# Performance work log

Measured on AMD Instinct MI355X. Metric: run time of the kernel, lower is better.

## Reference

```python
import jax, jax.numpy as jnp
import numpy as np

B, T, V, H, NH, NLVL = 64, 2048, 256, 64, 4, 2
HD = H // NH  # 16
EPS = 1e-5


def setup_inputs() -> dict:
    key = jax.random.key(0)
    ks = jax.random.split(key, 16)
    s = 0.05
    return {
        "x": jax.random.randint(ks[0], (B, T), 0, V),
        "emb": jax.random.normal(ks[1], (V, H), dtype=jnp.float32) * s,
        # LSTM params, PyTorch gate order i, f, g, o stacked along dim 0
        "w_ih": jax.random.normal(ks[2], (4 * H, H), dtype=jnp.float32) * s,
        "w_hh": jax.random.normal(ks[3], (4 * H, H), dtype=jnp.float32) * s,
        "b_ih": jax.random.normal(ks[4], (4 * H,), dtype=jnp.float32) * s,
        "b_hh": jax.random.normal(ks[5], (4 * H,), dtype=jnp.float32) * s,
        # two MHA levels, packed qkv in_proj like nn.MultiheadAttention
        "wqkv": jax.random.normal(ks[6], (NLVL, 3 * H, H), dtype=jnp.float32) * s,
        "bqkv": jax.random.normal(ks[7], (NLVL, 3 * H), dtype=jnp.float32) * s,
        "wo": jax.random.normal(ks[8], (NLVL, H, H), dtype=jnp.float32) * s,
        "bo": jax.random.normal(ks[9], (NLVL, H), dtype=jnp.float32) * s,
        "ln_g": jnp.ones((H,), dtype=jnp.float32),
        "ln_b": jnp.zeros((H,), dtype=jnp.float32),
        "fc_w": jax.random.normal(ks[10], (V, H), dtype=jnp.float32) * s,
        "fc_b": jax.random.normal(ks[11], (V,), dtype=jnp.float32) * s,
    }


def _lstm(x, w_ih, w_hh, b_ih, b_hh):
    # x: (B, T, H) -> (B, T, H); single layer, PyTorch gate order i,f,g,o
    b = x.shape[0]
    h0 = jnp.zeros((b, H), x.dtype)
    c0 = jnp.zeros((b, H), x.dtype)

    def step(carry, xt):
        h, c = carry
        g = xt @ w_ih.T + b_ih + h @ w_hh.T + b_hh  # (B, 4H)
        i, f, gg, o = jnp.split(g, 4, axis=-1)
        c = jax.nn.sigmoid(f) * c + jax.nn.sigmoid(i) * jnp.tanh(gg)
        h = jax.nn.sigmoid(o) * jnpp_tanh(c) if False else jax.nn.sigmoid(o) * jnp.tanh(c)
        return (h, c), h

    _, hs = jax.lax.scan(step, (h0, c0), jnp.swapaxes(x, 0, 1))  # (T, B, H)
    return jnp.swapaxes(hs, 0, 1)


def _mha(x, wqkv, bqkv, wo, bo):
    # Faithful to nn.MultiheadAttention with batch_first=False:
    # x: (L, N, E) where here L = batch dim of lstm_out, N = seq dim.
    L, N, E = x.shape
    qkv = x @ wqkv.T + bqkv  # (L, N, 3E)
    q, k, v = jnp.split(qkv, 3, axis=-1)
    q = q.reshape(L, N, NH, HD)
    k = k.reshape(L, N, NH, HD)
    v = v.reshape(L, N, NH, HD)
    scale = jnp.asarray(1.0 / np.sqrt(HD), x.dtype)
    att = jax.nn.softmax(jnp.einsum('lnhd,mnhd->nhlm', q, k) * scale, axis=-1)
    o = jnp.einsum('nhlm,mnhd->lnhd', att, v).reshape(L, N, E)
    return o @ wo.T + bo


def reference(x, emb, w_ih, w_hh, b_ih, b_hh, wqkv, bqkv, wo, bo, ln_g, ln_b, fc_w, fc_b):
    h = emb[x]  # (B, T, H)
    h = _lstm(h, w_ih, w_hh, b_ih, b_hh)  # (B, T, H)
    for l in range(NLVL):
        h = _mha(h, wqkv[l], bqkv[l], wo[l], bo[l])
    mu = jnp.mean(h, axis=-1, keepdims=True)
    var = jnp.mean(jnp.square(h - mu), axis=-1, keepdims=True)  # biased, like torch LN
    hn = (h - mu) * jax.lax.rsqrt(var + EPS) * ln_g + ln_b
    return hn @ fc_w.T + fc_b  # (B, T, V)
```

## Files before the change

### kernel.cpp

```cpp
#include <hip/hip_runtime.h>

enum { TT = 2048, HH = 64, BB = 64, GG = 256, VV = 256 };

static __device__ __forceinline__ void bar_lds(){
  asm volatile("s_waitcnt lgkmcnt(0)\n\ts_barrier" ::: "memory");
}

__global__ __launch_bounds__(256) void k_embw(const float* __restrict__ emb,
                                              const float* __restrict__ w_ih,
                                              const float* __restrict__ b_ih,
                                              const float* __restrict__ b_hh,
                                              float* __restrict__ embW){
  int v = blockIdx.x, g = threadIdx.x;
  __shared__ float e[HH];
  if (g < HH) e[g] = emb[v*HH + g];
  bar_lds();
  float acc = b_ih[g] + b_hh[g];
  const float* wr = w_ih + g*HH;
#pragma unroll
  for (int k = 0; k < HH; k += 4){
    float4 w4 = *(const float4*)(wr + k);
    acc = fmaf(e[k],   w4.x, acc); acc = fmaf(e[k+1], w4.y, acc);
    acc = fmaf(e[k+2], w4.z, acc); acc = fmaf(e[k+3], w4.w, acc);
  }
  embW[v*GG + g] = acc;
}

__global__ __launch_bounds__(256) void k_lstm(const int* __restrict__ x,
                                              const float* __restrict__ embW,
                                              const float* __restrict__ w_hh,
                                              float* __restrict__ hout){
  int b = blockIdx.x, g = threadIdx.x;
  __shared__ float hsh[HH];
  __shared__ float gsh[GG];
  float w[HH];
  {
    const float* wr = w_hh + g*HH;
#pragma unroll
    for (int k = 0; k < HH; k += 4)
      *(float4*)&w[k] = *(const float4*)(wr + k);
  }
  if (g < HH) hsh[g] = 0.f;
  float c = 0.f;
  const int* xb = x + b*TT;
  int i0 = xb[0];
  float gx = embW[i0*GG + g];
  int i1 = xb[1];
  const bool istanh = ((g >> 6) == 2);
  float* houtb = hout + (size_t)b*TT*HH;
  bar_lds();
#pragma unroll 2
  for (int t = 0; t < TT; t++){
    float gxn = embW[i1*GG + g];
    int inx = xb[(t + 2 < TT) ? (t + 2) : (TT - 1)];
    float a0 = 0.f, a1 = 0.f, a2 = 0.f, a3 = 0.f;
#pragma unroll
    for (int k = 0; k < 16; k += 4){
      float4 h0 = *(const float4*)&hsh[k];
      float4 h1 = *(const float4*)&hsh[16 + k];
      float4 h2 = *(const float4*)&hsh[32 + k];
      float4 h3 = *(const float4*)&hsh[48 + k];
      a0 = fmaf(w[k],      h0.x, a0); a0 = fmaf(w[k+1],    h0.y, a0);
      a0 = fmaf(w[k+2],    h0.z, a0); a0 = fmaf(w[k+3],    h0.w, a0);
      a1 = fmaf(w[16+k],   h1.x, a1); a1 = fmaf(w[16+k+1], h1.y, a1);
      a1 = fmaf(w[16+k+2], h1.z, a1); a1 = fmaf(w[16+k+3], h1.w, a1);
      a2 = fmaf(w[32+k],   h2.x, a2); a2 = fmaf(w[32+k+1], h2.y, a2);
      a2 = fmaf(w[32+k+2], h2.z, a2); a2 = fmaf(w[32+k+3], h2.w, a2);
      a3 = fmaf(w[48+k],   h3.x, a3); a3 = fmaf(w[48+k+1], h3.y, a3);
      a3 = fmaf(w[48+k+2], h3.z, a3); a3 = fmaf(w[48+k+3], h3.w, a3);
    }
    float acc = ((a0 + a1) + (a2 + a3)) + gx;
    float val;
    if (istanh) val = 1.f - 2.f/(__expf(2.f*acc) + 1.f);
    else        val = 1.f/(1.f + __expf(-acc));
    gsh[g] = val;
    bar_lds();
    if (g < HH){
      float i_ = gsh[g], f_ = gsh[HH+g], gg = gsh[128+g], o_ = gsh[192+g];
      c = fmaf(f_, c, i_*gg);
      float th = 1.f - 2.f/(__expf(2.f*c) + 1.f);
      float hv = o_*th;
      hsh[g] = hv;
      houtb[(size_t)t*HH + g] = hv;
    }
    bar_lds();
    gx = gxn; i1 = inx;
  }
}

__global__ __launch_bounds__(256) void k_mha(const float* __restrict__ hin,
                                             const float* __restrict__ wqkv,
                                             const float* __restrict__ bqkv,
                                             const float* __restrict__ wo,
                                             const float* __restrict__ bo,
                                             float* __restrict__ hout){
  int t = blockIdx.x, tid = threadIdx.x;
  __shared__ float xta[BB][HH];
  __shared__ float qkvs[BB][192];

  float wq[HH]; float bq = 0.f;
  if (tid < 192){
#pragma unroll
    for (int k = 0; k < HH; k += 4)
      *(float4*)&wq[k] = *(const float4*)(wqkv + tid*HH + k);
    bq = bqkv[tid];
  }
  {
    int r = tid >> 2, q = tid & 3;
    const float* p = hin + (size_t)(r*TT + t)*HH + q*16;
#pragma unroll
    for (int j = 0; j < 16; j += 4)
      *(float4*)&xta[r][q*16 + j] = *(const float4*)(p + j);
  }
  bar_lds();
  if (tid < 192){
#pragma unroll 4
    for (int b = 0; b < BB; b++){
      float acc = bq;
#pragma unroll
      for (int k = 0; k < HH; k += 4){
        float4 xv = *(const float4*)&xta[b][k];
        acc = fmaf(wq[k],   xv.x, acc); acc = fmaf(wq[k+1], xv.y, acc);
        acc = fmaf(wq[k+2], xv.z, acc); acc = fmaf(wq[k+3], xv.w, acc);
      }
      qkvs[b][tid] = acc;
    }
  }
  bar_lds();
  {
    int hd = tid >> 6, l = tid & 63;
    int qo = hd*16, ko = 64 + hd*16, vo = 128 + hd*16;
    float4 q0 = *(const float4*)&qkvs[l][qo];
    float4 q1 = *(const float4*)&qkvs[l][qo+4];
    float4 q2 = *(const float4*)&qkvs[l][qo+8];
    float4 q3 = *(const float4*)&qkvs[l][qo+12];
    float S[BB];
#pragma unroll
    for (int m = 0; m < BB; m++){
      float4 k0 = *(const float4*)&qkvs[m][ko];
      float4 k1 = *(const float4*)&qkvs[m][ko+4];
      float4 k2 = *(const float4*)&qkvs[m][ko+8];
      float4 k3 = *(const float4*)&qkvs[m][ko+12];
      float d;
      d = q0.x*k0.x;         d = fmaf(q0.y,k0.y,d); d = fmaf(q0.z,k0.z,d); d = fmaf(q0.w,k0.w,d);
      d = fmaf(q1.x,k1.x,d); d = fmaf(q1.y,k1.y,d); d = fmaf(q1.z,k1.z,d); d = fmaf(q1.w,k1.w,d);
      d = fmaf(q2.x,k2.x,d); d = fmaf(q2.y,k2.y,d); d = fmaf(q2.z,k2.z,d); d = fmaf(q2.w,k2.w,d);
      d = fmaf(q3.x,k3.x,d); d = fmaf(q3.y,k3.y,d); d = fmaf(q3.z,k3.z,d); d = fmaf(q3.w,k3.w,d);
      S[m] = 0.25f*d;
    }
    float mx = S[0];
#pragma unroll
    for (int m = 1; m < BB; m++) mx = fmaxf(mx, S[m]);
    float sum = 0.f;
#pragma unroll
    for (int m = 0; m < BB; m++){ S[m] = __expf(S[m] - mx); sum += S[m]; }
    float inv = 1.f/sum;
    float4 a0 = make_float4(0,0,0,0), a1 = a0, a2 = a0, a3 = a0;
#pragma unroll
    for (int m = 0; m < BB; m++){
      float s = S[m];
      float4 v0 = *(const float4*)&qkvs[m][vo];
      float4 v1 = *(const float4*)&qkvs[m][vo+4];
      float4 v2 = *(const float4*)&qkvs[m][vo+8];
      float4 v3 = *(const float4*)&qkvs[m][vo+12];
      a0.x = fmaf(s,v0.x,a0.x); a0.y = fmaf(s,v0.y,a0.y); a0.z = fmaf(s,v0.z,a0.z); a0.w = fmaf(s,v0.w,a0.w);
      a1.x = fmaf(s,v1.x,a1.x); a1.y = fmaf(s,v1.y,a1.y); a1.z = fmaf(s,v1.z,a1.z); a1.w = fmaf(s,v1.w,a1.w);
      a2.x = fmaf(s,v2.x,a2.x); a2.y = fmaf(s,v2.y,a2.y); a2.z = fmaf(s,v2.z,a2.z); a2.w = fmaf(s,v2.w,a2.w);
      a3.x = fmaf(s,v3.x,a3.x); a3.y = fmaf(s,v3.y,a3.y); a3.z = fmaf(s,v3.z,a3.z); a3.w = fmaf(s,v3.w,a3.w);
    }
    a0.x*=inv; a0.y*=inv; a0.z*=inv; a0.w*=inv;
    a1.x*=inv; a1.y*=inv; a1.z*=inv; a1.w*=inv;
    a2.x*=inv; a2.y*=inv; a2.z*=inv; a2.w*=inv;
    a3.x*=inv; a3.y*=inv; a3.z*=inv; a3.w*=inv;
    bar_lds();
    *(float4*)&xta[l][qo]    = a0;
    *(float4*)&xta[l][qo+4]  = a1;
    *(float4*)&xta[l][qo+8]  = a2;
    *(float4*)&xta[l][qo+12] = a3;
  }
  bar_lds();
  {
    int c = tid & 63, wg = tid >> 6;
    float wor[HH];
#pragma unroll
    for (int k = 0; k < HH; k += 4)
      *(float4*)&wor[k] = *(const float4*)(wo + c*HH + k);
    float bo4 = bo[c];
#pragma unroll 2
    for (int j = 0; j < 16; j++){
      int b = wg*16 + j;
      float acc = bo4;
#pragma unroll
      for (int k = 0; k < HH; k += 4){
        float4 xv = *(const float4*)&xta[b][k];
        acc = fmaf(wor[k],   xv.x, acc); acc = fmaf(wor[k+1], xv.y, acc);
        acc = fmaf(wor[k+2], xv.z, acc); acc = fmaf(wor[k+3], xv.w, acc);
      }
      hout[(size_t)(b*TT + t)*HH + c] = acc;
    }
  }
}

__global__ __launch_bounds__(256) void k_fc(const float* __restrict__ hin,
                                            const float* __restrict__ ln_g,
                                            const float* __restrict__ ln_b,
                                            const float* __restrict__ fc_w,
                                            const float* __restrict__ fc_b,
                                            float* __restrict__ out){
  int tid = threadIdx.x;
  __shared__ float tile[64][68];
  __shared__ float ps[64][4];
  __shared__ float pq[64][4];
  __shared__ float mu[64], rs[64];
  float w[HH];
  float wsum = 0.f, bias2 = fc_b[tid];
#pragma unroll
  for (int k = 0; k < HH; k += 4){
    float4 wv = *(const float4*)(fc_w + tid*HH + k);
    float4 gv = *(const float4*)(ln_g + k);
    float4 bv = *(const float4*)(ln_b + k);
    bias2 = fmaf(bv.x, wv.x, bias2); bias2 = fmaf(bv.y, wv.y, bias2);
    bias2 = fmaf(bv.z, wv.z, bias2); bias2 = fmaf(bv.w, wv.w, bias2);
    w[k]   = gv.x*wv.x; w[k+1] = gv.y*wv.y;
    w[k+2] = gv.z*wv.z; w[k+3] = gv.w*wv.w;
    wsum += w[k] + w[k+1] + w[k+2] + w[k+3];
  }
  int r = tid >> 2, q = tid & 3;
  for (int ti = 0; ti < 4; ti++){
    int rowbase = blockIdx.x*256 + ti*64;
    const float* p = hin + (size_t)(rowbase + r)*HH + q*16;
    float xv[16];
#pragma unroll
    for (int j = 0; j < 16; j += 4)
      *(float4*)&xv[j] = *(const float4*)(p + j);
    float s1 = 0.f, s2 = 0.f;
#pragma unroll
    for (int j = 0; j < 16; j++){ s1 += xv[j]; s2 = fmaf(xv[j], xv[j], s2); }
#pragma unroll
    for (int j = 0; j < 16; j += 4)
      *(float4*)&tile[r][q*16 + j] = *(const float4*)&xv[j];
    ps[r][q] = s1; pq[r][q] = s2;
    bar_lds();
    if (tid < 64){
      float4 a  = *(const float4*)&ps[tid][0];
      float4 b4 = *(const float4*)&pq[tid][0];
      float m = (a.x + a.y + a.z + a.w) * (1.f/64.f);
      float v = (b4.x + b4.y + b4.z + b4.w) * (1.f/64.f) - m*m;
      mu[tid] = m;
      rs[tid] = rsqrtf(v + 1e-5f);
    }
    bar_lds();
#pragma unroll 2
    for (int rr = 0; rr < 64; rr++){
      float acc = 0.f;
#pragma unroll
      for (int k = 0; k < HH; k += 4){
        float4 x4 = *(const float4*)&tile[rr][k];
        acc = fmaf(w[k],   x4.x, acc); acc = fmaf(w[k+1], x4.y, acc);
        acc = fmaf(w[k+2], x4.z, acc); acc = fmaf(w[k+3], x4.w, acc);
      }
      float o = rs[rr]*(acc - mu[rr]*wsum) + bias2;
      out[(size_t)(rowbase + rr)*VV + tid] = o;
    }
    bar_lds();
  }
}

extern "C" void kernel_launch(void* const* d_in, const int* in_sizes, int n_in,
                              void* d_out, int out_size, void* d_ws, size_t ws_size,
                              hipStream_t stream){
  (void)in_sizes; (void)n_in; (void)out_size; (void)ws_size;
  const int*   x    = (const int*)d_in[0];
  const float* emb  = (const float*)d_in[1];
  const float* w_ih = (const float*)d_in[2];
  const float* w_hh = (const float*)d_in[3];
  const float* b_ih = (const float*)d_in[4];
  const float* b_hh = (const float*)d_in[5];
  const float* wqkv = (const float*)d_in[6];
  const float* bqkv = (const float*)d_in[7];
  const float* wo   = (const float*)d_in[8];
  const float* bo   = (const float*)d_in[9];
  const float* ln_g = (const float*)d_in[10];
  const float* ln_b = (const float*)d_in[11];
  const float* fc_w = (const float*)d_in[12];
  const float* fc_b = (const float*)d_in[13];

  char* ws = (char*)d_ws;
  float* embW = (float*)ws;
  float* bufA = (float*)(ws + (1<<20));
  float* bufB = bufA + (size_t)BB*TT*HH;

  k_embw<<<VV,  256, 0, stream>>>(emb, w_ih, b_ih, b_hh, embW);
  k_lstm<<<BB,  256, 0, stream>>>(x, embW, w_hh, bufA);
  k_mha <<<TT,  256, 0, stream>>>(bufA, wqkv,          bqkv,       wo,          bo,      bufB);
  k_mha <<<TT,  256, 0, stream>>>(bufB, wqkv + 192*64, bqkv + 192, wo + 64*64,  bo + 64, bufA);
  k_fc  <<<512, 256, 0, stream>>>(bufA, ln_g, ln_b, fc_w, fc_b, (float*)d_out);
}
```

Baseline: 1.775 ms.

## Batch 16 LSTM sequences per block and use bf16 MFMA for recurrence

The LSTM recurrence now processes 16 batch rows per block and computes the hidden-to-gate matmul with bf16 MFMA 16x16x32 instructions. The input-gate contribution seeds the accumulator. The weights are held as bf16 fragments in registers and the hidden state as bf16 in LDS. Each thread handles all four gates for its rows, which removes the gate-exchange barrier, but only 4 blocks are launched instead of 64. This trades parallelism across CUs and fp32 precision in the recurrent matmul for fewer serialized per-step instructions.

```diff
diff --git a/kernel.cpp b/kernel.cpp
--- a/kernel.cpp
+++ b/kernel.cpp
@@ -1,9 +1,24 @@
 #include <hip/hip_runtime.h>
 
 enum { TT = 2048, HH = 64, BB = 64, GG = 256, VV = 256 };
+
+typedef __attribute__((ext_vector_type(8))) short bf16x8;
+typedef __attribute__((ext_vector_type(4))) float f32x4;
 
 static __device__ __forceinline__ void bar_lds(){
   asm volatile("s_waitcnt lgkmcnt(0)\n\ts_barrier" ::: "memory");
+}
+
+static __device__ __forceinline__ unsigned short f2bs(float f){
+  unsigned int u = __builtin_bit_cast(unsigned int, f);
+  u += 0x7fffu + ((u >> 16) & 1u);
+  return (unsigned short)(u >> 16);
+}
+static __device__ __forceinline__ bf16x8 pack8(const float* v){
+  union { unsigned short s[8]; bf16x8 v8; } u;
+#pragma unroll
+  for (int i = 0; i < 8; i++) u.s[i] = f2bs(v[i]);
+  return u.v8;
 }
 
 __global__ __launch_bounds__(256) void k_embw(const float* __restrict__ emb,
@@ -30,61 +45,84 @@
                                               const float* __restrict__ embW,
                                               const float* __restrict__ w_hh,
                                               float* __restrict__ hout){
-  int b = blockIdx.x, g = threadIdx.x;
-  __shared__ float hsh[HH];
-  __shared__ float gsh[GG];
-  float w[HH];
+  const int tid  = threadIdx.x;
+  const int q    = tid >> 6;
+  const int lane = tid & 63;
+  const int n    = lane & 15;
+  const int quad = lane >> 4;
+  const int j    = blockIdx.x*16 + n;
+
+  __shared__ __attribute__((aligned(16))) unsigned short h_lds[16][72];
+
+  for (int idx = tid; idx < 16*72; idx += 256) ((unsigned short*)h_lds)[idx] = 0;
+
+  bf16x8 A[4][2];
+#pragma unroll
+  for (int G = 0; G < 4; G++){
+    const int grow = G*64 + q*16 + (lane & 15);
+#pragma unroll
+    for (int kc = 0; kc < 2; kc++){
+      float tmp[8];
+      const float* src = w_hh + grow*HH + kc*32 + quad*8;
+      *(float4*)&tmp[0] = *(const float4*)src;
+      *(float4*)&tmp[4] = *(const float4*)(src + 4);
+      A[G][kc] = pack8(tmp);
+    }
+  }
+
+  const int* xrow = x + j*TT;
+  int v_nxt = xrow[1];
+  const int erow = q*16 + quad*4;
+  f32x4 gx[4];
   {
-    const float* wr = w_hh + g*HH;
-#pragma unroll
-    for (int k = 0; k < HH; k += 4)
-      *(float4*)&w[k] = *(const float4*)(wr + k);
-  }
-  if (g < HH) hsh[g] = 0.f;
-  float c = 0.f;
-  const int* xb = x + b*TT;
-  int i0 = xb[0];
-  float gx = embW[i0*GG + g];
-  int i1 = xb[1];
-  const bool istanh = ((g >> 6) == 2);
-  float* houtb = hout + (size_t)b*TT*HH;
-  bar_lds();
-#pragma unroll 2
+    int v0 = xrow[0];
+#pragma unroll
+    for (int G = 0; G < 4; G++)
+      gx[G] = *(const f32x4*)(embW + v0*GG + G*64 + erow);
+  }
+  float cs[4] = {0.f, 0.f, 0.f, 0.f};
+  float* hb = hout + (size_t)j*TT*HH + erow;
+
+  bar_lds();
+
   for (int t = 0; t < TT; t++){
-    float gxn = embW[i1*GG + g];
-    int inx = xb[(t + 2 < TT) ? (t + 2) : (TT - 1)];
-    float a0 = 0.f, a1 = 0.f, a2 = 0.f, a3 = 0.f;
-#pragma unroll
-    for (int k = 0; k < 16; k += 4){
-      float4 h0 = *(const float4*)&hsh[k];
-      float4 h1 = *(const float4*)&hsh[16 + k];
-      float4 h2 = *(const float4*)&hsh[32 + k];
-      float4 h3 = *(const float4*)&hsh[48 + k];
-      a0 = fmaf(w[k],      h0.x, a0); a0 = fmaf(w[k+1],    h0.y, a0);
-      a0 = fmaf(w[k+2],    h0.z, a0); a0 = fmaf(w[k+3],    h0.w, a0);
-      a1 = fmaf(w[16+k],   h1.x, a1); a1 = fmaf(w[16+k+1], h1.y, a1);
-      a1 = fmaf(w[16+k+2], h1.z, a1); a1 = fmaf(w[16+k+3], h1.w, a1);
-      a2 = fmaf(w[32+k],   h2.x, a2); a2 = fmaf(w[32+k+1], h2.y, a2);
-      a2 = fmaf(w[32+k+2], h2.z, a2); a2 = fmaf(w[32+k+3], h2.w, a2);
-      a3 = fmaf(w[48+k],   h3.x, a3); a3 = fmaf(w[48+k+1], h3.y, a3);
-      a3 = fmaf(w[48+k+2], h3.z, a3); a3 = fmaf(w[48+k+3], h3.w, a3);
-    }
-    float acc = ((a0 + a1) + (a2 + a3)) + gx;
-    float val;
-    if (istanh) val = 1.f - 2.f/(__expf(2.f*acc) + 1.f);
-    else        val = 1.f/(1.f + __expf(-acc));
-    gsh[g] = val;
-    bar_lds();
-    if (g < HH){
-      float i_ = gsh[g], f_ = gsh[HH+g], gg = gsh[128+g], o_ = gsh[192+g];
-      c = fmaf(f_, c, i_*gg);
-      float th = 1.f - 2.f/(__expf(2.f*c) + 1.f);
-      float hv = o_*th;
-      hsh[g] = hv;
-      houtb[(size_t)t*HH + g] = hv;
-    }
-    bar_lds();
-    gx = gxn; i1 = inx;
+    f32x4 gxn[4];
+#pragma unroll
+    for (int G = 0; G < 4; G++)
+      gxn[G] = *(const f32x4*)(embW + v_nxt*GG + G*64 + erow);
+    int v_nn = xrow[(t + 2 < TT) ? (t + 2) : (TT - 1)];
+
+    bf16x8 B0 = *(const bf16x8*)&h_lds[n][quad*8];
+    bf16x8 B1 = *(const bf16x8*)&h_lds[n][32 + quad*8];
+
+    f32x4 acc[4];
+#pragma unroll
+    for (int G = 0; G < 4; G++){
+      acc[G] = __builtin_amdgcn_mfma_f32_16x16x32_bf16(A[G][0], B0, gx[G],   0, 0, 0);
+      acc[G] = __builtin_amdgcn_mfma_f32_16x16x32_bf16(A[G][1], B1, acc[G],  0, 0, 0);
+    }
+
+    float hn[4];
+#pragma unroll
+    for (int r = 0; r < 4; r++){
+      float i_ = 1.f/(1.f + __expf(-acc[0][r]));
+      float f_ = 1.f/(1.f + __expf(-acc[1][r]));
+      float g_ = 1.f - 2.f/(__expf(2.f*acc[2][r]) + 1.f);
+      float o_ = 1.f/(1.f + __expf(-acc[3][r]));
+      cs[r] = fmaf(f_, cs[r], i_*g_);
+      hn[r] = o_*(1.f - 2.f/(__expf(2.f*cs[r]) + 1.f));
+    }
+
+    *(float4*)(hb + (size_t)t*HH) = make_float4(hn[0], hn[1], hn[2], hn[3]);
+    bar_lds();
+    unsigned int p0 = (unsigned int)f2bs(hn[0]) | ((unsigned int)f2bs(hn[1]) << 16);
+    unsigned int p1 = (unsigned int)f2bs(hn[2]) | ((unsigned int)f2bs(hn[3]) << 16);
+    *(uint2*)&h_lds[n][erow] = make_uint2(p0, p1);
+    bar_lds();
+
+#pragma unroll
+    for (int G = 0; G < 4; G++) gx[G] = gxn[G];
+    v_nxt = v_nn;
   }
 }
 
@@ -109,8 +147,8 @@
     int r = tid >> 2, q = tid & 3;
     const float* p = hin + (size_t)(r*TT + t)*HH + q*16;
 #pragma unroll
-    for (int j = 0; j < 16; j += 4)
-      *(float4*)&xta[r][q*16 + j] = *(const float4*)(p + j);
+    for (int jj = 0; jj < 16; jj += 4)
+      *(float4*)&xta[r][q*16 + jj] = *(const float4*)(p + jj);
   }
   bar_lds();
   if (tid < 192){
@@ -187,8 +225,8 @@
       *(float4*)&wor[k] = *(const float4*)(wo + c*HH + k);
     float bo4 = bo[c];
 #pragma unroll 2
-    for (int j = 0; j < 16; j++){
-      int b = wg*16 + j;
+    for (int jj = 0; jj < 16; jj++){
+      int b = wg*16 + jj;
       float acc = bo4;
 #pragma unroll
       for (int k = 0; k < HH; k += 4){
@@ -231,14 +269,14 @@
     const float* p = hin + (size_t)(rowbase + r)*HH + q*16;
     float xv[16];
 #pragma unroll
-    for (int j = 0; j < 16; j += 4)
-      *(float4*)&xv[j] = *(const float4*)(p + j);
+    for (int jj = 0; jj < 16; jj += 4)
+      *(float4*)&xv[jj] = *(const float4*)(p + jj);
     float s1 = 0.f, s2 = 0.f;
 #pragma unroll
-    for (int j = 0; j < 16; j++){ s1 += xv[j]; s2 = fmaf(xv[j], xv[j], s2); }
-#pragma unroll
-    for (int j = 0; j < 16; j += 4)
-      *(float4*)&tile[r][q*16 + j] = *(const float4*)&xv[j];
+    for (int jj = 0; jj < 16; jj++){ s1 += xv[jj]; s2 = fmaf(xv[jj], xv[jj], s2); }
+#pragma unroll
+    for (int jj = 0; jj < 16; jj += 4)
+      *(float4*)&tile[r][q*16 + jj] = *(const float4*)&xv[jj];
     ps[r][q] = s1; pq[r][q] = s2;
     bar_lds();
     if (tid < 64){
@@ -290,9 +328,9 @@
   float* bufA = (float*)(ws + (1<<20));
   float* bufB = bufA + (size_t)BB*TT*HH;
 
-  k_embw<<<VV,  256, 0, stream>>>(emb, w_ih, b_ih, b_hh, embW);
-  k_lstm<<<BB,  256, 0, stream>>>(x, embW, w_hh, bufA);
-  k_mha <<<TT,  256, 0, stream>>>(bufA, wqkv,          bqkv,       wo,          bo,      bufB);
-  k_mha <<<TT,  256, 0, stream>>>(bufB, wqkv + 192*64, bqkv + 192, wo + 64*64,  bo + 64, bufA);
-  k_fc  <<<512, 256, 0, stream>>>(bufA, ln_g, ln_b, fc_w, fc_b, (float*)d_out);
-}
+  k_embw<<<VV,    256, 0, stream>>>(emb, w_ih, b_ih, b_hh, embW);
+  k_lstm<<<BB/16, 256, 0, stream>>>(x, embW, w_hh, bufA);
+  k_mha <<<TT,    256, 0, stream>>>(bufA, wqkv,          bqkv,       wo,         bo,      bufB);
+  k_mha <<<TT,    256, 0, stream>>>(bufB, wqkv + 192*64, bqkv + 192, wo + 64*64, bo + 64, bufA);
+  k_fc  <<<512,   256, 0, stream>>>(bufA, ln_g, ln_b, fc_w, fc_b, (float*)d_out);
+}
```

Measured after the change: 2.508 ms. 41.3% more time.
